# Performance work log

Hardware: AMD Instinct MI355X
Metric: run time of the kernel (lower is better)

The kernel has to match this reference:

```python
import jax, jax.numpy as jnp
import numpy as np

CH = 256
IC = 128  # inter_channels = channels // reduction
TEMP = 0.05


def setup_inputs() -> dict:
    key = jax.random.key(0)
    k1, k2, k3, k4, k5 = jax.random.split(key, 5)
    x = jax.random.normal(k1, (8, CH, 64, 64), dtype=jnp.float32)
    # 1x1 conv weights stored as [out_ch, in_ch]
    w_qkv = jax.random.normal(k2, (3 * IC, CH), dtype=jnp.float32) * 0.01
    b_qkv = jax.random.normal(k3, (3 * IC,), dtype=jnp.float32) * 0.01
    w_out = jax.random.normal(k4, (CH, IC), dtype=jnp.float32) * 0.01
    b_out = jax.random.normal(k5, (CH,), dtype=jnp.float32) * 0.01
    return {"x": x, "w_qkv": w_qkv, "b_qkv": b_qkv, "w_out": w_out, "b_out": b_out}


def reference(x, w_qkv, b_qkv, w_out, b_out):
    b, c, h, w = x.shape
    n = h * w
    ic = w_qkv.shape[0] // 3
    # 1x1 conv QKV projection
    qkv = jnp.einsum('bchw,oc->bohw', x, w_qkv) + b_qkv[None, :, None, None]
    qkv = qkv.reshape(b, 3, ic, n)
    q, k, v = qkv[:, 0], qkv[:, 1], qkv[:, 2]  # each [b, ic, n]
    # mean-center q and k over spatial positions (per channel)
    k = k - k.mean(axis=-1, keepdims=True)
    q = q - q.mean(axis=-1, keepdims=True)
    # pairwise_weight[b, i, j] = sum_c k[b, c, i] * q[b, c, j]
    pw = jnp.einsum('bci,bcj->bij', k, q)
    pw = pw / jnp.sqrt(jnp.float32(ic))  # use_scale=True
    pw = pw / TEMP
    pw = jax.nn.softmax(pw, axis=-1)  # [b, n, n]
    # y[b, c, i] = sum_j pw[b, i, j] * v[b, c, j]
    y = jnp.einsum('bij,bcj->bci', pw, v).reshape(b, ic, h, w)
    out = x + jnp.einsum('bchw,oc->bohw', y, w_out) + b_out[None, :, None, None]
    return out
```

## Files before the change

### kernel.cpp

```cpp
#include <hip/hip_runtime.h>
#include <hip/hip_bf16.h>

typedef __bf16 bf16_t;
typedef __bf16 bf16x8 __attribute__((ext_vector_type(8)));
typedef float f32x4 __attribute__((ext_vector_type(4)));
typedef float f32x16 __attribute__((ext_vector_type(16)));

#define MFMA16(a, b, c) __builtin_amdgcn_mfma_f32_16x16x32_bf16((a), (b), (c), 0, 0, 0)
#define MFMA32(a, b, c) __builtin_amdgcn_mfma_f32_32x32x16_bf16((a), (b), (c), 0, 0, 0)

constexpr int BATCH = 8, CH = 256, IC = 128, NPOS = 4096;
constexpr float SM_C = 2.5503488f;

constexpr size_t OFF_XT    = 0;
constexpr size_t OFF_QT    = 16777216;
constexpr size_t OFF_KT    = 25165824;
constexpr size_t OFF_V     = 33554432;
constexpr size_t OFF_WQKV  = 41943040;
constexpr size_t OFF_WOUT  = 42139648;
constexpr size_t OFF_XMEAN = 42205184;
constexpr size_t OFF_QKM   = 42213376;
constexpr size_t OFF_PL    = 42221568;

__device__ __forceinline__ void gload_lds16(const char* g, char* lds) {
    __builtin_amdgcn_global_load_lds((const __attribute__((address_space(1))) unsigned int*)g,
                                     (__attribute__((address_space(3))) unsigned int*)lds, 16, 0,
                                     0);
}
__device__ __forceinline__ float fexp2(float x) {
    float r;
    asm("v_exp_f32 %0, %1" : "=v"(r) : "v"(x));
    return r;
}
__device__ __forceinline__ int cvtpk(float lo, float hi) {
    int r;
    asm("v_cvt_pk_bf16_f32 %0, %1, %2" : "=v"(r) : "v"(lo), "v"(hi));
    return r;
}

__global__ void k_convert_w(const float* __restrict__ wqkv, const float* __restrict__ wout,
                            bf16_t* __restrict__ wqkv_b, bf16_t* __restrict__ wout_b) {
    int idx = blockIdx.x * 256 + threadIdx.x;
    if (idx < 384 * 256) wqkv_b[idx] = (bf16_t)wqkv[idx];
    int j = idx - 384 * 256;
    if (j >= 0 && j < 256 * 128) wout_b[j] = (bf16_t)wout[j];
}

__global__ void k_xmean(const float* __restrict__ x, float* __restrict__ xmean) {
    int c = blockIdx.x, b = blockIdx.y;
    const float4* xv = (const float4*)(x + ((size_t)(b * CH + c)) * NPOS);
    float s = 0.f;
#pragma unroll
    for (int r = 0; r < 4; r++) {
        float4 v = xv[r * 256 + threadIdx.x];
        s += v.x + v.y + v.z + v.w;
    }
    __shared__ float red[256];
    red[threadIdx.x] = s;
    __syncthreads();
    for (int st = 128; st > 0; st >>= 1) {
        if (threadIdx.x < st) red[threadIdx.x] += red[threadIdx.x + st];
        __syncthreads();
    }
    if (threadIdx.x == 0) xmean[b * CH + c] = red[0] * (1.0f / NPOS);
}

__global__ void k_qkmean(const float* __restrict__ wqkv, const float* __restrict__ xmean,
                         float* __restrict__ qkm) {
    int o = blockIdx.x, b = blockIdx.y, lane = threadIdx.x;
    float4 w = ((const float4*)(wqkv + (size_t)o * CH))[lane];
    float4 xm = ((const float4*)(xmean + b * CH))[lane];
    float s = w.x * xm.x + w.y * xm.y + w.z * xm.z + w.w * xm.w;
#pragma unroll
    for (int m = 1; m < 64; m <<= 1) s += __shfl_xor(s, m, 64);
    if (lane == 0) qkm[b * CH + o] = s;
}

__global__ void k_transpose(const float* __restrict__ x, bf16_t* __restrict__ xt) {
    __shared__ float t[32][33];
    int p0 = blockIdx.x * 32, c0 = blockIdx.y * 32, b = blockIdx.z;
    int i = threadIdx.x >> 5, j = threadIdx.x & 31;
#pragma unroll
    for (int q = 0; q < 4; q++) {
        int c = c0 + q * 8 + i;
        t[q * 8 + i][j] = x[((size_t)(b * CH + c)) * NPOS + p0 + j];
    }
    __syncthreads();
#pragma unroll
    for (int q = 0; q < 4; q++) {
        int p = p0 + q * 8 + i;
        xt[((size_t)(b * NPOS + p)) * CH + c0 + j] = (bf16_t)t[j][q * 8 + i];
    }
}

__global__ __launch_bounds__(256, 2) void k_qkv(const bf16_t* __restrict__ xt,
                                                const bf16_t* __restrict__ wqkv_b,
                                                const float* __restrict__ qkm,
                                                const float* __restrict__ b_qkv,
                                                bf16_t* __restrict__ qt, bf16_t* __restrict__ kt,
                                                bf16_t* __restrict__ v) {
    int bid = blockIdx.x;
    int b = bid & 7;
    int r0 = bid >> 3;
    int sec = r0 % 3;
    int pt = r0 / 3;
    int p0 = pt * 128;
    int wid = threadIdx.x >> 6, lane = threadIdx.x & 63;
    int g = lane >> 4, li = lane & 15;
    int wr = wid >> 1, wc = wid & 1;
    f32x4 acc[4][4] = {};
    if (sec < 2) {
        int ob = sec * 128;
#pragma unroll 1
        for (int kk = 0; kk < 8; kk++) {
            bf16x8 af[4], bfg[4];
#pragma unroll
            for (int fa = 0; fa < 4; fa++) {
                int p = p0 + wr * 64 + fa * 16 + li;
                af[fa] = *(const bf16x8*)(xt + ((size_t)(b * NPOS + p)) * CH + kk * 32 + g * 8);
            }
#pragma unroll
            for (int fb = 0; fb < 4; fb++) {
                int o = ob + wc * 64 + fb * 16 + li;
                bfg[fb] = *(const bf16x8*)(wqkv_b + (size_t)o * CH + kk * 32 + g * 8);
            }
#pragma unroll
            for (int fa = 0; fa < 4; fa++)
#pragma unroll
                for (int fb = 0; fb < 4; fb++) acc[fa][fb] = MFMA16(af[fa], bfg[fb], acc[fa][fb]);
        }
        bf16_t* dst = (sec == 0) ? qt : kt;
        float scale = (sec == 1) ? SM_C : 1.0f;
#pragma unroll
        for (int fb = 0; fb < 4; fb++) {
            int ol = wc * 64 + fb * 16 + li;
            float mean = qkm[b * CH + sec * 128 + ol];
#pragma unroll
            for (int fa = 0; fa < 4; fa++)
#pragma unroll
                for (int r = 0; r < 4; r++) {
                    int p = p0 + wr * 64 + fa * 16 + g * 4 + r;
                    dst[((size_t)(b * NPOS + p)) * IC + ol] =
                        (bf16_t)((acc[fa][fb][r] - mean) * scale);
                }
        }
    } else {
#pragma unroll 1
        for (int kk = 0; kk < 8; kk++) {
            bf16x8 af[4], bfg[4];
#pragma unroll
            for (int fa = 0; fa < 4; fa++) {
                int o = 256 + wr * 64 + fa * 16 + li;
                af[fa] = *(const bf16x8*)(wqkv_b + (size_t)o * CH + kk * 32 + g * 8);
            }
#pragma unroll
            for (int fb = 0; fb < 4; fb++) {
                int p = p0 + wc * 64 + fb * 16 + li;
                bfg[fb] = *(const bf16x8*)(xt + ((size_t)(b * NPOS + p)) * CH + kk * 32 + g * 8);
            }
#pragma unroll
            for (int fa = 0; fa < 4; fa++)
#pragma unroll
                for (int fb = 0; fb < 4; fb++) acc[fa][fb] = MFMA16(af[fa], bfg[fb], acc[fa][fb]);
        }
#pragma unroll
        for (int fa = 0; fa < 4; fa++)
#pragma unroll
            for (int r = 0; r < 4; r++) {
                int oe = wr * 64 + fa * 16 + g * 4 + r;
                float bias = b_qkv[256 + oe];
#pragma unroll
                for (int fb = 0; fb < 4; fb++) {
                    int p = p0 + wc * 64 + fb * 16 + li;
                    v[((size_t)(b * IC + oe)) * NPOS + p] = (bf16_t)(acc[fa][fb][r] + bias);
                }
            }
    }
}

constexpr int TJ = 64;

__global__ __launch_bounds__(256, 2) void k_attn(const bf16_t* __restrict__ qt,
                                                 const bf16_t* __restrict__ kt,
                                                 const bf16_t* __restrict__ v,
                                                 bf16_t* __restrict__ pacc,
                                                 float* __restrict__ pl) {
    __shared__ __attribute__((aligned(128))) char smem[2 * 32768];
    const int bid = blockIdx.x;
    const int b = bid & 7;
    const int r0 = bid >> 3;
    const int jh = r0 & 1;
    const int it = r0 >> 1;
    const int jbase = jh * 2048;
    const int wid = threadIdx.x >> 6, lane = threadIdx.x & 63;
    const int col = lane & 31, h = lane >> 5;
    const int iw0 = it * 128 + wid * 32;
    const bf16_t* ktb = kt + (size_t)b * NPOS * IC;
    const bf16_t* qtb = qt + (size_t)b * NPOS * IC;
    const bf16_t* vb = v + (size_t)b * IC * NPOS;

    int qoff_[4], voff_[4];
#pragma unroll
    for (int u = 0; u < 4; u++) {
        int t = wid * 4 + u;
        int qrow = 4 * t + (lane >> 4);
        qoff_[u] = qrow * 256 + (((lane & 15) ^ (qrow & 7)) << 4);
        int vrow = 8 * t + (lane >> 3);
        voff_[u] = vrow * 8192 + (((lane & 7) ^ (vrow & 7)) << 4);
    }

    auto stage = [&](int dstpar, int sj) {
        const char* qs = (const char*)qtb + (size_t)sj * 256;
        const char* vs = (const char*)vb + (size_t)sj * 2;
        char* qd = smem + dstpar * 32768;
        char* vd = qd + 16384;
#pragma unroll
        for (int u = 0; u < 4; u++) {
            gload_lds16(qs + qoff_[u], qd + (wid * 4 + u) * 1024);
            gload_lds16(vs + voff_[u], vd + (wid * 4 + u) * 1024);
        }
    };

    stage(0, jbase);

    bf16x8 bk[8];
#pragma unroll
    for (int ks = 0; ks < 8; ks++)
        bk[ks] = *(const bf16x8*)(ktb + (size_t)(iw0 + col) * IC + ks * 16 + h * 8);

    f32x16 acc[4] = {};
    float ls[4] = {0.f, 0.f, 0.f, 0.f};

    auto body = [&](int par, int nextj) {
        stage(par ^ 1, nextj);
        asm volatile("s_waitcnt vmcnt(8)" ::: "memory");
        __builtin_amdgcn_s_barrier();
        asm volatile("" ::: "memory");
        const char* qb = smem + par * 32768;
        const char* vbuf = qb + 16384;
#pragma unroll
        for (int jsub = 0; jsub < 2; jsub++) {
            f32x16 s = {};
#pragma unroll
            for (int ks = 0; ks < 8; ks++) {
                bf16x8 aq = *(const bf16x8*)(qb + (jsub * 32 + col) * 256 +
                                             (((ks * 2 + h) ^ (col & 7)) << 4));
                s = MFMA32(aq, bk[ks], s);
            }
            float e[16];
#pragma unroll
            for (int r = 0; r < 16; r++) e[r] = fexp2(s[r]);
#pragma unroll
            for (int r = 0; r < 16; r++) ls[r & 3] += e[r];
            int w[8];
#pragma unroll
            for (int q = 0; q < 8; q++) w[q] = cvtpk(e[2 * q], e[2 * q + 1]);
            asm("v_permlane32_swap_b32 %0, %1" : "+v"(w[0]), "+v"(w[2]));
            asm("v_permlane32_swap_b32 %0, %1" : "+v"(w[1]), "+v"(w[3]));
            asm("v_permlane32_swap_b32 %0, %1" : "+v"(w[4]), "+v"(w[6]));
            asm("v_permlane32_swap_b32 %0, %1" : "+v"(w[5]), "+v"(w[7]));
            union {
                int u[4];
                bf16x8 v;
            } pb0, pb1;
            pb0.u[0] = w[0]; pb0.u[1] = w[1]; pb0.u[2] = w[2]; pb0.u[3] = w[3];
            pb1.u[0] = w[4]; pb1.u[1] = w[5]; pb1.u[2] = w[6]; pb1.u[3] = w[7];
#pragma unroll
            for (int kl = 0; kl < 2; kl++) {
                int kg = jsub * 2 + kl;
                bf16x8 pbf = kl == 0 ? pb0.v : pb1.v;
#pragma unroll
                for (int cs = 0; cs < 4; cs++) {
                    bf16x8 av = *(const bf16x8*)(vbuf + (cs * 32 + col) * 128 +
                                                 (((kg * 2 + h) ^ (col & 7)) << 4));
                    acc[cs] = MFMA32(av, pbf, acc[cs]);
                }
            }
        }
        asm volatile("" ::: "memory");
        __builtin_amdgcn_s_barrier();
    };

#pragma unroll 1
    for (int jo = 0; jo < 2048; jo += 2 * TJ) {
        body(0, jbase + ((jo + TJ) & 2047));
        body(1, jbase + ((jo + 2 * TJ) & 2047));
    }

    float lsum = (ls[0] + ls[1]) + (ls[2] + ls[3]);
    lsum += __shfl_xor(lsum, 32, 64);
    const int i = iw0 + col;
    if (h == 0) pl[((size_t)(b * 2 + jh)) * NPOS + i] = lsum;

    bf16_t* po = pacc + ((size_t)(b * 2 + jh)) * NPOS * IC;
#pragma unroll
    for (int cs = 0; cs < 4; cs++)
#pragma unroll
        for (int q = 0; q < 8; q++) {
            int u = cvtpk(acc[cs][2 * q], acc[cs][2 * q + 1]);
            int c0 = cs * 32 + ((q & 1) << 1) + ((q >> 1) << 3) + 4 * h;
            *(int*)((char*)po + ((size_t)i * IC + c0) * 2) = u;
        }
}

__global__ void k_merge(const bf16_t* __restrict__ pacc, const float* __restrict__ pl,
                        bf16_t* __restrict__ yt) {
    int idx = blockIdx.x * 256 + threadIdx.x;
    int co = idx & 15;
    int i = (idx >> 4) & 4095;
    int b = idx >> 16;
    const bf16x8* p0 = (const bf16x8*)pacc + ((size_t)(b * 2 + 0) * NPOS + i) * 16 + co;
    const bf16x8* p1 = (const bf16x8*)pacc + ((size_t)(b * 2 + 1) * NPOS + i) * 16 + co;
    float l = pl[(size_t)(b * 2 + 0) * NPOS + i] + pl[(size_t)(b * 2 + 1) * NPOS + i];
    float inv = 1.0f / l;
    bf16x8 a0 = *p0, a1 = *p1, o;
#pragma unroll
    for (int j = 0; j < 8; j++) o[j] = (bf16_t)(((float)a0[j] + (float)a1[j]) * inv);
    *((bf16x8*)yt + ((size_t)b * NPOS + i) * 16 + co) = o;
}

__global__ __launch_bounds__(256, 2) void k_out(const bf16_t* __restrict__ yt,
                                                const bf16_t* __restrict__ wout_b,
                                                const float* __restrict__ x,
                                                const float* __restrict__ b_out,
                                                float* __restrict__ out) {
    int bid = blockIdx.x;
    int b = bid & 7;
    int r0 = bid >> 3;
    int oct = r0 & 1, pt = r0 >> 1;
    int p0 = pt * 128, oc0 = oct * 128;
    int wid = threadIdx.x >> 6, lane = threadIdx.x & 63;
    int g = lane >> 4, li = lane & 15;
    int wr = wid >> 1, wc = wid & 1;
    f32x4 acc[4][4] = {};
#pragma unroll
    for (int kk = 0; kk < 4; kk++) {
        bf16x8 af[4], bfg[4];
#pragma unroll
        for (int fa = 0; fa < 4; fa++) {
            int oc = oc0 + wr * 64 + fa * 16 + li;
            af[fa] = *(const bf16x8*)(wout_b + (size_t)oc * IC + kk * 32 + g * 8);
        }
#pragma unroll
        for (int fb = 0; fb < 4; fb++) {
            int p = p0 + wc * 64 + fb * 16 + li;
            bfg[fb] = *(const bf16x8*)(yt + ((size_t)(b * NPOS + p)) * IC + kk * 32 + g * 8);
        }
#pragma unroll
        for (int fa = 0; fa < 4; fa++)
#pragma unroll
            for (int fb = 0; fb < 4; fb++) acc[fa][fb] = MFMA16(af[fa], bfg[fb], acc[fa][fb]);
    }
#pragma unroll
    for (int fa = 0; fa < 4; fa++)
#pragma unroll
        for (int r = 0; r < 4; r++) {
            int oc = oc0 + wr * 64 + fa * 16 + g * 4 + r;
            float bias = b_out[oc];
#pragma unroll
            for (int fb = 0; fb < 4; fb++) {
                int p = p0 + wc * 64 + fb * 16 + li;
                size_t idx = ((size_t)(b * CH + oc)) * NPOS + p;
                out[idx] = acc[fa][fb][r] + x[idx] + bias;
            }
        }
}

extern "C" void kernel_launch(void* const* d_in, const int* in_sizes, int n_in, void* d_out,
                              int out_size, void* d_ws, size_t ws_size, hipStream_t stream) {
    const float* x = (const float*)d_in[0];
    const float* w_qkv = (const float*)d_in[1];
    const float* b_qkv = (const float*)d_in[2];
    const float* w_out = (const float*)d_in[3];
    const float* b_out = (const float*)d_in[4];
    float* out = (float*)d_out;
    char* ws = (char*)d_ws;

    bf16_t* xt = (bf16_t*)(ws + OFF_XT);
    bf16_t* pacc = (bf16_t*)(ws + OFF_XT);
    bf16_t* qt = (bf16_t*)(ws + OFF_QT);
    bf16_t* kt = (bf16_t*)(ws + OFF_KT);
    bf16_t* yt = (bf16_t*)(ws + OFF_KT);
    bf16_t* v = (bf16_t*)(ws + OFF_V);
    bf16_t* wqkv_b = (bf16_t*)(ws + OFF_WQKV);
    bf16_t* wout_b = (bf16_t*)(ws + OFF_WOUT);
    float* xmean = (float*)(ws + OFF_XMEAN);
    float* qkm = (float*)(ws + OFF_QKM);
    float* pl = (float*)(ws + OFF_PL);

    k_convert_w<<<512, 256, 0, stream>>>(w_qkv, w_out, wqkv_b, wout_b);
    k_xmean<<<dim3(256, 8), 256, 0, stream>>>(x, xmean);
    k_qkmean<<<dim3(256, 8), 64, 0, stream>>>(w_qkv, xmean, qkm);
    k_transpose<<<dim3(128, 8, 8), 256, 0, stream>>>(x, xt);
    k_qkv<<<768, 256, 0, stream>>>(xt, wqkv_b, qkm, b_qkv, qt, kt, v);
    k_attn<<<512, 256, 0, stream>>>(qt, kt, v, pacc, pl);
    k_merge<<<2048, 256, 0, stream>>>(pacc, pl, yt);
    k_out<<<512, 256, 0, stream>>>(yt, wout_b, x, b_out, out);
}
```

Before: 149.2 us.

## Merge prep kernels, fold split merge into output GEMM, retune attention swizzle and priority

Four small preprocessing kernels become two combined launches, and the separate merge pass is folded into the output projection, which now reads both partial accumulators and normalizes on the fly. This cuts launch overhead and one full intermediate write/read. The attention kernel gets a wider 16-way LDS XOR swizzle with a different V tile layout, plus s_setprio around the MFMA sections to favor matrix issue. The cost is redundant normalization math in k_out, and the changed V staging layout has to line up exactly with the new reads.

```diff
diff --git a/kernel.cpp b/kernel.cpp
--- a/kernel.cpp
+++ b/kernel.cpp
@@ -9,7 +9,7 @@
 #define MFMA16(a, b, c) __builtin_amdgcn_mfma_f32_16x16x32_bf16((a), (b), (c), 0, 0, 0)
 #define MFMA32(a, b, c) __builtin_amdgcn_mfma_f32_32x32x16_bf16((a), (b), (c), 0, 0, 0)
 
-constexpr int BATCH = 8, CH = 256, IC = 128, NPOS = 4096;
+constexpr int CH = 256, IC = 128, NPOS = 4096;
 constexpr float SM_C = 2.5503488f;
 
 constexpr size_t OFF_XT    = 0;
@@ -38,16 +38,19 @@
     return r;
 }
 
-__global__ void k_convert_w(const float* __restrict__ wqkv, const float* __restrict__ wout,
-                            bf16_t* __restrict__ wqkv_b, bf16_t* __restrict__ wout_b) {
-    int idx = blockIdx.x * 256 + threadIdx.x;
-    if (idx < 384 * 256) wqkv_b[idx] = (bf16_t)wqkv[idx];
-    int j = idx - 384 * 256;
-    if (j >= 0 && j < 256 * 128) wout_b[j] = (bf16_t)wout[j];
-}
-
-__global__ void k_xmean(const float* __restrict__ x, float* __restrict__ xmean) {
-    int c = blockIdx.x, b = blockIdx.y;
+__global__ void k_prep0(const float* __restrict__ wqkv, const float* __restrict__ wout,
+                        const float* __restrict__ x, bf16_t* __restrict__ wqkv_b,
+                        bf16_t* __restrict__ wout_b, float* __restrict__ xmean) {
+    int bid = blockIdx.x;
+    if (bid < 512) {
+        int idx = bid * 256 + threadIdx.x;
+        if (idx < 384 * 256) wqkv_b[idx] = (bf16_t)wqkv[idx];
+        int j = idx - 384 * 256;
+        if (j >= 0 && j < 256 * 128) wout_b[j] = (bf16_t)wout[j];
+        return;
+    }
+    int xbid = bid - 512;
+    int c = xbid & 255, b = xbid >> 8;
     const float4* xv = (const float4*)(x + ((size_t)(b * CH + c)) * NPOS);
     float s = 0.f;
 #pragma unroll
@@ -65,20 +68,24 @@
     if (threadIdx.x == 0) xmean[b * CH + c] = red[0] * (1.0f / NPOS);
 }
 
-__global__ void k_qkmean(const float* __restrict__ wqkv, const float* __restrict__ xmean,
-                         float* __restrict__ qkm) {
-    int o = blockIdx.x, b = blockIdx.y, lane = threadIdx.x;
-    float4 w = ((const float4*)(wqkv + (size_t)o * CH))[lane];
-    float4 xm = ((const float4*)(xmean + b * CH))[lane];
-    float s = w.x * xm.x + w.y * xm.y + w.z * xm.z + w.w * xm.w;
-#pragma unroll
-    for (int m = 1; m < 64; m <<= 1) s += __shfl_xor(s, m, 64);
-    if (lane == 0) qkm[b * CH + o] = s;
-}
-
-__global__ void k_transpose(const float* __restrict__ x, bf16_t* __restrict__ xt) {
+__global__ void k_prep1(const float* __restrict__ x, const float* __restrict__ wqkv,
+                        const float* __restrict__ xmean, bf16_t* __restrict__ xt,
+                        float* __restrict__ qkm) {
+    int bid = blockIdx.x;
+    if (bid >= 8192) {
+        int xbid = bid - 8192;
+        int wid = threadIdx.x >> 6, lane = threadIdx.x & 63;
+        int o = (xbid & 63) * 4 + wid, b = xbid >> 6;
+        float4 w = ((const float4*)(wqkv + (size_t)o * CH))[lane];
+        float4 xm = ((const float4*)(xmean + b * CH))[lane];
+        float s = w.x * xm.x + w.y * xm.y + w.z * xm.z + w.w * xm.w;
+#pragma unroll
+        for (int m = 1; m < 64; m <<= 1) s += __shfl_xor(s, m, 64);
+        if (lane == 0) qkm[b * CH + o] = s;
+        return;
+    }
     __shared__ float t[32][33];
-    int p0 = blockIdx.x * 32, c0 = blockIdx.y * 32, b = blockIdx.z;
+    int p0 = (bid & 127) * 32, c0 = ((bid >> 7) & 7) * 32, b = bid >> 10;
     int i = threadIdx.x >> 5, j = threadIdx.x & 31;
 #pragma unroll
     for (int q = 0; q < 4; q++) {
@@ -204,9 +211,10 @@
     for (int u = 0; u < 4; u++) {
         int t = wid * 4 + u;
         int qrow = 4 * t + (lane >> 4);
-        qoff_[u] = qrow * 256 + (((lane & 15) ^ (qrow & 7)) << 4);
-        int vrow = 8 * t + (lane >> 3);
-        voff_[u] = vrow * 8192 + (((lane & 7) ^ (vrow & 7)) << 4);
+        qoff_[u] = qrow * 256 + (((lane & 15) ^ (qrow & 15)) << 4);
+        int crow = 4 * t + (lane >> 4);
+        int src = (lane & 15) ^ (crow & 15);
+        voff_[u] = (crow + (src >> 3) * 64) * 8192 + (src & 7) * 16;
     }
 
     auto stage = [&](int dstpar, int sj) {
@@ -241,12 +249,14 @@
 #pragma unroll
         for (int jsub = 0; jsub < 2; jsub++) {
             f32x16 s = {};
+            __builtin_amdgcn_s_setprio(1);
 #pragma unroll
             for (int ks = 0; ks < 8; ks++) {
                 bf16x8 aq = *(const bf16x8*)(qb + (jsub * 32 + col) * 256 +
-                                             (((ks * 2 + h) ^ (col & 7)) << 4));
+                                             (((ks * 2 + h) ^ (col & 15)) << 4));
                 s = MFMA32(aq, bk[ks], s);
             }
+            __builtin_amdgcn_s_setprio(0);
             float e[16];
 #pragma unroll
             for (int r = 0; r < 16; r++) e[r] = fexp2(s[r]);
@@ -265,17 +275,20 @@
             } pb0, pb1;
             pb0.u[0] = w[0]; pb0.u[1] = w[1]; pb0.u[2] = w[2]; pb0.u[3] = w[3];
             pb1.u[0] = w[4]; pb1.u[1] = w[5]; pb1.u[2] = w[6]; pb1.u[3] = w[7];
+            __builtin_amdgcn_s_setprio(1);
 #pragma unroll
             for (int kl = 0; kl < 2; kl++) {
                 int kg = jsub * 2 + kl;
                 bf16x8 pbf = kl == 0 ? pb0.v : pb1.v;
 #pragma unroll
                 for (int cs = 0; cs < 4; cs++) {
-                    bf16x8 av = *(const bf16x8*)(vbuf + (cs * 32 + col) * 128 +
-                                                 (((kg * 2 + h) ^ (col & 7)) << 4));
+                    int crow = (cs & 1) * 32 + col;
+                    int p = ((cs >> 1) * 8 + kg * 2 + h) ^ (crow & 15);
+                    bf16x8 av = *(const bf16x8*)(vbuf + crow * 256 + (p << 4));
                     acc[cs] = MFMA32(av, pbf, acc[cs]);
                 }
             }
+            __builtin_amdgcn_s_setprio(0);
         }
         asm volatile("" ::: "memory");
         __builtin_amdgcn_s_barrier();
@@ -303,23 +316,8 @@
         }
 }
 
-__global__ void k_merge(const bf16_t* __restrict__ pacc, const float* __restrict__ pl,
-                        bf16_t* __restrict__ yt) {
-    int idx = blockIdx.x * 256 + threadIdx.x;
-    int co = idx & 15;
-    int i = (idx >> 4) & 4095;
-    int b = idx >> 16;
-    const bf16x8* p0 = (const bf16x8*)pacc + ((size_t)(b * 2 + 0) * NPOS + i) * 16 + co;
-    const bf16x8* p1 = (const bf16x8*)pacc + ((size_t)(b * 2 + 1) * NPOS + i) * 16 + co;
-    float l = pl[(size_t)(b * 2 + 0) * NPOS + i] + pl[(size_t)(b * 2 + 1) * NPOS + i];
-    float inv = 1.0f / l;
-    bf16x8 a0 = *p0, a1 = *p1, o;
-#pragma unroll
-    for (int j = 0; j < 8; j++) o[j] = (bf16_t)(((float)a0[j] + (float)a1[j]) * inv);
-    *((bf16x8*)yt + ((size_t)b * NPOS + i) * 16 + co) = o;
-}
-
-__global__ __launch_bounds__(256, 2) void k_out(const bf16_t* __restrict__ yt,
+__global__ __launch_bounds__(256, 2) void k_out(const bf16_t* __restrict__ pacc,
+                                                const float* __restrict__ pl,
                                                 const bf16_t* __restrict__ wout_b,
                                                 const float* __restrict__ x,
                                                 const float* __restrict__ b_out,
@@ -332,6 +330,14 @@
     int wid = threadIdx.x >> 6, lane = threadIdx.x & 63;
     int g = lane >> 4, li = lane & 15;
     int wr = wid >> 1, wc = wid & 1;
+    const bf16_t* pa0 = pacc + (size_t)(b * 2 + 0) * NPOS * IC;
+    const bf16_t* pa1 = pacc + (size_t)(b * 2 + 1) * NPOS * IC;
+    float inv[4];
+#pragma unroll
+    for (int fb = 0; fb < 4; fb++) {
+        int p = p0 + wc * 64 + fb * 16 + li;
+        inv[fb] = 1.0f / (pl[(size_t)(b * 2 + 0) * NPOS + p] + pl[(size_t)(b * 2 + 1) * NPOS + p]);
+    }
     f32x4 acc[4][4] = {};
 #pragma unroll
     for (int kk = 0; kk < 4; kk++) {
@@ -344,7 +350,11 @@
 #pragma unroll
         for (int fb = 0; fb < 4; fb++) {
             int p = p0 + wc * 64 + fb * 16 + li;
-            bfg[fb] = *(const bf16x8*)(yt + ((size_t)(b * NPOS + p)) * IC + kk * 32 + g * 8);
+            bf16x8 a0 = *(const bf16x8*)(pa0 + (size_t)p * IC + kk * 32 + g * 8);
+            bf16x8 a1 = *(const bf16x8*)(pa1 + (size_t)p * IC + kk * 32 + g * 8);
+#pragma unroll
+            for (int e = 0; e < 8; e++)
+                bfg[fb][e] = (bf16_t)(((float)a0[e] + (float)a1[e]) * inv[fb]);
         }
 #pragma unroll
         for (int fa = 0; fa < 4; fa++)
@@ -380,7 +390,6 @@
     bf16_t* pacc = (bf16_t*)(ws + OFF_XT);
     bf16_t* qt = (bf16_t*)(ws + OFF_QT);
     bf16_t* kt = (bf16_t*)(ws + OFF_KT);
-    bf16_t* yt = (bf16_t*)(ws + OFF_KT);
     bf16_t* v = (bf16_t*)(ws + OFF_V);
     bf16_t* wqkv_b = (bf16_t*)(ws + OFF_WQKV);
     bf16_t* wout_b = (bf16_t*)(ws + OFF_WOUT);
@@ -388,12 +397,9 @@
     float* qkm = (float*)(ws + OFF_QKM);
     float* pl = (float*)(ws + OFF_PL);
 
-    k_convert_w<<<512, 256, 0, stream>>>(w_qkv, w_out, wqkv_b, wout_b);
-    k_xmean<<<dim3(256, 8), 256, 0, stream>>>(x, xmean);
-    k_qkmean<<<dim3(256, 8), 64, 0, stream>>>(w_qkv, xmean, qkm);
-    k_transpose<<<dim3(128, 8, 8), 256, 0, stream>>>(x, xt);
+    k_prep0<<<2560, 256, 0, stream>>>(w_qkv, w_out, x, wqkv_b, wout_b, xmean);
+    k_prep1<<<8704, 256, 0, stream>>>(x, w_qkv, xmean, xt, qkm);
     k_qkv<<<768, 256, 0, stream>>>(xt, wqkv_b, qkm, b_qkv, qt, kt, v);
     k_attn<<<512, 256, 0, stream>>>(qt, kt, v, pacc, pl);
-    k_merge<<<2048, 256, 0, stream>>>(pacc, pl, yt);
-    k_out<<<512, 256, 0, stream>>>(yt, wout_b, x, b_out, out);
-}
+    k_out<<<512, 256, 0, stream>>>(pacc, pl, wout_b, x, b_out, out);
+}
```

Measured after the change: 142.1 us. -4.7%, faster.
